# Kernel optimization log

Measured on AMD Instinct MI355X. Metric: run time of the kernel, lower is better.

## Reference

```python
import jax, jax.numpy as jnp
import numpy as np

NUM_HEADS = 12
HEAD_DIM = 64  # d_out // num_heads = 768 // 12


def setup_inputs() -> dict:
    key = jax.random.key(0)
    k1, k2 = jax.random.split(key)
    x = jax.random.normal(k1, (2, 2048, 768), dtype=jnp.float32)
    # torch Linear weight: [d_out, d_in], y = x @ W.T
    Wq = jax.random.normal(k2, (768, 768), dtype=jnp.float32) * 0.02
    return {"x": x, "Wq": Wq}


def reference(x, Wq):
    b, n, d_in = x.shape
    H, hd = NUM_HEADS, HEAD_DIM
    d_out = H * hd
    # NOTE: the original module uses Wq for queries, keys AND values.
    qkv = x @ Wq.T                                   # [b, n, d_out]
    h = qkv.reshape(b, n, H, hd).transpose(0, 2, 1, 3)  # [b, H, n, hd]
    scores = jnp.einsum('bhqd,bhkd->bhqk', h, h)      # [b, H, n, n]
    causal = jnp.triu(jnp.ones((n, n), dtype=bool), k=1)
    scores = jnp.where(causal, -jnp.inf, scores)
    attn = jax.nn.softmax(scores / jnp.sqrt(jnp.float32(hd)), axis=-1)
    ctx = jnp.einsum('bhqk,bhkd->bhqd', attn, h)      # [b, H, n, hd]
    # faithful to source: transpose(-2,-1) -> [b, H, hd, n], then view(b, n, d_out)
    ctx = ctx.transpose(0, 1, 3, 2)
    return ctx.reshape(b, n, d_out)
```

## Files before the change

### kernel.cpp

```cpp
#include <hip/hip_runtime.h>
#include <math.h>

typedef __attribute__((ext_vector_type(8)))  short short8;
typedef __attribute__((ext_vector_type(4)))  float floatx4;
typedef __attribute__((ext_vector_type(16))) float floatx16;

#define MFMA16(a, b, c) __builtin_amdgcn_mfma_f32_16x16x32_bf16(a, b, c, 0, 0, 0)
#define MFMA32(a, b, c) __builtin_amdgcn_mfma_f32_32x32x16_bf16(a, b, c, 0, 0, 0)

constexpr int NSEQ = 2048;
constexpr int DIN  = 768;
constexpr int NH   = 12;
constexpr float QSCALE = 0.18033688011112042f;

constexpr int PK = 72;

__device__ __forceinline__ ushort f2bf(float f) {
    unsigned u = __float_as_uint(f);
    u += 0x7FFF + ((u >> 16) & 1);
    return (ushort)(u >> 16);
}
__device__ __forceinline__ float bf2f(ushort u) {
    return __uint_as_float(((unsigned)u) << 16);
}
__device__ __forceinline__ unsigned cvt_pk_bf16(float lo, float hi) {
    unsigned r;
    asm("v_cvt_pk_bf16_f32 %0, %1, %2" : "=v"(r) : "v"(lo), "v"(hi));
    return r;
}
__device__ __forceinline__ short8 pk8(float4 a, float4 b) {
    union { unsigned u[4]; short8 s; } r;
    r.u[0] = cvt_pk_bf16(a.x, a.y);
    r.u[1] = cvt_pk_bf16(a.z, a.w);
    r.u[2] = cvt_pk_bf16(b.x, b.y);
    r.u[3] = cvt_pk_bf16(b.z, b.w);
    return r.s;
}
__device__ __forceinline__ void bar_lds() {
    asm volatile("s_waitcnt lgkmcnt(0)" ::: "memory");
    __builtin_amdgcn_s_barrier();
}

__global__ __launch_bounds__(256, 3)
void qkv_mfma(const float* __restrict__ x, const float* __restrict__ Wq,
              ushort* __restrict__ h)
{
    __shared__ ushort As[2][64 * PK];
    __shared__ ushort Bs[2][64 * PK];

    const int tid  = threadIdx.x;
    const int w    = tid >> 6;
    const int lane = tid & 63;
    const int m    = lane & 15;
    const int quad = lane >> 4;
    const int r0   = blockIdx.x * 64;
    const int c0   = blockIdx.y * 64;
    const int mrow0 = (w & 1) * 32;
    const int ncol0 = (w >> 1) * 32;

    const int srow = tid >> 3;
    const int scol = (tid & 7) * 8;

    floatx4 C[2][2] = {};
    float4 arf[2][2], brf[2][2];

    #pragma unroll
    for (int i = 0; i < 2; ++i) {
        const float* ax = x  + (size_t)(r0 + srow + i * 32) * DIN + scol;
        const float* bx = Wq + (size_t)(c0 + srow + i * 32) * DIN + scol;
        arf[i][0] = ((const float4*)ax)[0]; arf[i][1] = ((const float4*)ax)[1];
        brf[i][0] = ((const float4*)bx)[0]; brf[i][1] = ((const float4*)bx)[1];
    }
    #pragma unroll
    for (int i = 0; i < 2; ++i) {
        *(short8*)&As[0][(srow + i * 32) * PK + scol] = pk8(arf[i][0], arf[i][1]);
        *(short8*)&Bs[0][(srow + i * 32) * PK + scol] = pk8(brf[i][0], brf[i][1]);
    }
    #pragma unroll
    for (int i = 0; i < 2; ++i) {
        const float* ax = x  + (size_t)(r0 + srow + i * 32) * DIN + 64 + scol;
        const float* bx = Wq + (size_t)(c0 + srow + i * 32) * DIN + 64 + scol;
        arf[i][0] = ((const float4*)ax)[0]; arf[i][1] = ((const float4*)ax)[1];
        brf[i][0] = ((const float4*)bx)[0]; brf[i][1] = ((const float4*)bx)[1];
    }
    bar_lds();

    for (int kk = 0; kk < 12; ++kk) {
        const int cur = kk & 1;

        #pragma unroll
        for (int kt2 = 0; kt2 < 2; ++kt2) {
            short8 a0 = *(const short8*)&As[cur][(mrow0 + m)      * PK + kt2 * 32 + quad * 8];
            short8 a1 = *(const short8*)&As[cur][(mrow0 + 16 + m) * PK + kt2 * 32 + quad * 8];
            short8 b0 = *(const short8*)&Bs[cur][(ncol0 + m)      * PK + kt2 * 32 + quad * 8];
            short8 b1 = *(const short8*)&Bs[cur][(ncol0 + 16 + m) * PK + kt2 * 32 + quad * 8];
            C[0][0] = MFMA16(a0, b0, C[0][0]);
            C[0][1] = MFMA16(a0, b1, C[0][1]);
            C[1][0] = MFMA16(a1, b0, C[1][0]);
            C[1][1] = MFMA16(a1, b1, C[1][1]);
        }

        if (kk + 1 < 12) {
            const int nxt = cur ^ 1;
            #pragma unroll
            for (int i = 0; i < 2; ++i) {
                *(short8*)&As[nxt][(srow + i * 32) * PK + scol] = pk8(arf[i][0], arf[i][1]);
                *(short8*)&Bs[nxt][(srow + i * 32) * PK + scol] = pk8(brf[i][0], brf[i][1]);
            }
            if (kk + 2 < 12) {
                const int k0 = (kk + 2) * 64;
                #pragma unroll
                for (int i = 0; i < 2; ++i) {
                    const float* ax = x  + (size_t)(r0 + srow + i * 32) * DIN + k0 + scol;
                    const float* bx = Wq + (size_t)(c0 + srow + i * 32) * DIN + k0 + scol;
                    arf[i][0] = ((const float4*)ax)[0]; arf[i][1] = ((const float4*)ax)[1];
                    brf[i][0] = ((const float4*)bx)[0]; brf[i][1] = ((const float4*)bx)[1];
                }
            }
            bar_lds();
        }
    }

    #pragma unroll
    for (int mt = 0; mt < 2; ++mt)
        #pragma unroll
        for (int nt = 0; nt < 2; ++nt) {
            int cg = c0 + ncol0 + nt * 16 + m;
            int head = cg >> 6, d = cg & 63;
            #pragma unroll
            for (int r = 0; r < 4; ++r) {
                int rg = r0 + mrow0 + mt * 16 + quad * 4 + r;
                int b = rg >> 11, q = rg & 2047;
                h[((size_t)(b * NH + head) * NSEQ + q) * 64 + d] = f2bf(C[mt][nt][r]);
            }
        }
}

__global__ __launch_bounds__(128, 3)
void attn_mfma(const ushort* __restrict__ h, float* __restrict__ out)
{
    __shared__ ushort Ks[64 * PK];
    __shared__ ushort Vt[64 * PK];

    const int tid  = threadIdx.x;
    const int w    = tid >> 6;
    const int lane = tid & 63;
    const int col  = lane & 31;
    const int hi   = lane >> 5;

    const int xi = blockIdx.x;
    const int bh = blockIdx.y;
    const int qt = ((bh >> 2) & 1) ? xi : (63 - xi);
    const int q0 = qt * 32;
    const int nkt = (qt >> 1) + 1;
    const ushort* __restrict__ Hh = h + (size_t)bh * NSEQ * 64;

    const int kp = (tid & 15) * 4;
    const int cc = tid >> 4;

    short8 qa[4];
    #pragma unroll
    for (int s = 0; s < 4; ++s) {
        short8 raw = *(const short8*)(Hh + (size_t)(q0 + col) * 64 + s * 16 + hi * 8);
        #pragma unroll
        for (int j = 0; j < 8; ++j)
            qa[s][j] = (short)f2bf(bf2f((ushort)raw[j]) * QSCALE);
    }

    floatx16 O[2] = {};
    float lacc = 0.0f;

    short8 fr[4];
#define PREFETCH(KT) do {                                                      \
    const ushort* s_ = Hh + ((size_t)(KT) * 64 + kp) * 64 + cc * 8;            \
    fr[0] = *(const short8*)s_;                                                \
    fr[1] = *(const short8*)(s_ + 64);                                         \
    fr[2] = *(const short8*)(s_ + 128);                                        \
    fr[3] = *(const short8*)(s_ + 192);                                        \
} while (0)

    PREFETCH(0);

    for (int kt = 0; kt < nkt; ++kt) {
        bar_lds();

        #pragma unroll
        for (int j = 0; j < 4; ++j) {
            int ky = kp + j;
            *(short8*)&Ks[ky * PK + (((cc + 2 * (ky & 7)) & 7) << 3)] = fr[j];
        }
        {
            union { short8 v; ushort u[8]; } f0, f1, f2, f3;
            f0.v = fr[0]; f1.v = fr[1]; f2.v = fr[2]; f3.v = fr[3];
            #pragma unroll
            for (int i = 0; i < 8; ++i) {
                uint2 dw;
                dw.x = (unsigned)f0.u[i] | ((unsigned)f1.u[i] << 16);
                dw.y = (unsigned)f2.u[i] | ((unsigned)f3.u[i] << 16);
                *(uint2*)&Vt[(cc * 8 + i) * PK + kp] = dw;
            }
        }
        if (kt + 1 < nkt) PREFETCH(kt + 1);
        bar_lds();

        floatx16 S = {};
        #pragma unroll
        for (int s = 0; s < 4; ++s) {
            int key = w * 32 + col;
            short8 ka = *(const short8*)
                &Ks[key * PK + (((s * 2 + hi + 2 * (col & 7)) & 7) << 3)];
            S = MFMA32(ka, qa[s], S);
        }

        const bool diag = (kt == nkt - 1);
        const int kbase = kt * 64 + w * 32;
        const int qabs  = q0 + col;
        unsigned bfr[2][4];
        #pragma unroll
        for (int h2 = 0; h2 < 2; ++h2) {
            float p[8];
            #pragma unroll
            for (int j = 0; j < 8; ++j) {
                const int reg = h2 * 8 + j;
                const int kl  = (reg & 3) + 8 * (reg >> 2) + 4 * hi;
                float pv = exp2f(S[reg]);
                if (diag && (kbase + kl > qabs)) pv = 0.0f;
                p[j] = pv;
                lacc += pv;
            }
            unsigned a0 = cvt_pk_bf16(p[0], p[1]);
            unsigned a1 = cvt_pk_bf16(p[2], p[3]);
            unsigned a2 = cvt_pk_bf16(p[4], p[5]);
            unsigned a3 = cvt_pk_bf16(p[6], p[7]);
            asm volatile("v_permlane32_swap_b32 %0, %1" : "+v"(a0), "+v"(a2));
            asm volatile("v_permlane32_swap_b32 %0, %1" : "+v"(a1), "+v"(a3));
            bfr[h2][0] = a0; bfr[h2][1] = a1; bfr[h2][2] = a2; bfr[h2][3] = a3;
        }

        #pragma unroll
        for (int h2 = 0; h2 < 2; ++h2) {
            union { unsigned u[4]; short8 v; } pb;
            pb.u[0] = bfr[h2][0]; pb.u[1] = bfr[h2][1];
            pb.u[2] = bfr[h2][2]; pb.u[3] = bfr[h2][3];
            #pragma unroll
            for (int dt = 0; dt < 2; ++dt) {
                short8 va = *(const short8*)
                    &Vt[(dt * 32 + col) * PK + w * 32 + h2 * 16 + hi * 8];
                O[dt] = MFMA32(va, pb.v, O[dt]);
            }
        }
    }
#undef PREFETCH

    lacc += __shfl_xor(lacc, 32);

    float* OmA = (float*)&Ks[0];
    float* OmB = OmA + 32 * 33;
    float* Lg  = OmB + 32 * 33;

    bar_lds();
    {
        float* Om = (w == 0) ? OmA : OmB;
        #pragma unroll
        for (int reg = 0; reg < 16; ++reg) {
            const int dl = (reg & 3) + 8 * (reg >> 2) + 4 * hi;
            Om[dl * 33 + col] = (w == 0) ? O[1][reg] : O[0][reg];
        }
        if (hi == 0) Lg[w * 32 + col] = lacc;
    }
    bar_lds();
    {
        const float linv = 1.0f / (Lg[col] + Lg[32 + col]);
        float* Om = (w == 0) ? OmB : OmA;
        #pragma unroll
        for (int reg = 0; reg < 16; ++reg) {
            const int dl = (reg & 3) + 8 * (reg >> 2) + 4 * hi;
            const int d  = w * 32 + dl;
            const float v = ((w == 0) ? O[0][reg] : O[1][reg]) + Om[dl * 33 + col];
            out[((size_t)bh * 64 + d) * NSEQ + q0 + col] = v * linv;
        }
    }
}

extern "C" void kernel_launch(void* const* d_in, const int* in_sizes, int n_in,
                              void* d_out, int out_size, void* d_ws, size_t ws_size,
                              hipStream_t stream)
{
    (void)in_sizes; (void)n_in; (void)out_size; (void)ws_size;
    const float* x  = (const float*)d_in[0];
    const float* Wq = (const float*)d_in[1];
    float* out = (float*)d_out;

    ushort* hb = (ushort*)d_ws;

    qkv_mfma<<<dim3(64, 12), dim3(256), 0, stream>>>(x, Wq, hb);
    attn_mfma<<<dim3(64, 24), dim3(128), 0, stream>>>(hb, out);
}
```

Baseline: 119.6 us.

## Pair causal query tiles per block and widen key tiles to 128

Each attention block now processes two query tiles (qt and 63-qt) in sequence, so every block gets the same total causal work, and the grid shrinks to 32x24. Key tiles grow from 64 to 128 rows, so each warp computes two 32-key sub-tiles per iteration, with new swizzled LDS layouts for K and transposed V (PV stride 136). The cross-warp reduction at the end is rewritten so warp 1 hands its partial output to warp 0, which does the final normalization. The aim is to balance load and halve barrier and LDS fill overhead per key. In exchange LDS use roughly doubles, which may lower occupancy, and there are half as many blocks.

After: 144.4 us. +20.7%, slower.

```diff
diff --git a/kernel.cpp b/kernel.cpp
--- a/kernel.cpp
+++ b/kernel.cpp
@@ -14,6 +14,7 @@
 constexpr float QSCALE = 0.18033688011112042f;
 
 constexpr int PK = 72;
+constexpr int PV = 136;
 
 __device__ __forceinline__ ushort f2bf(float f) {
     unsigned u = __float_as_uint(f);
@@ -139,8 +140,8 @@
 __global__ __launch_bounds__(128, 3)
 void attn_mfma(const ushort* __restrict__ h, float* __restrict__ out)
 {
-    __shared__ ushort Ks[64 * PK];
-    __shared__ ushort Vt[64 * PK];
+    __shared__ ushort Ks[128 * PK];
+    __shared__ ushort Vt[64 * PV];
 
     const int tid  = threadIdx.x;
     const int w    = tid >> 6;
@@ -148,138 +149,164 @@
     const int col  = lane & 31;
     const int hi   = lane >> 5;
 
-    const int xi = blockIdx.x;
+    const int p  = blockIdx.x;
     const int bh = blockIdx.y;
-    const int qt = ((bh >> 2) & 1) ? xi : (63 - xi);
-    const int q0 = qt * 32;
-    const int nkt = (qt >> 1) + 1;
     const ushort* __restrict__ Hh = h + (size_t)bh * NSEQ * 64;
 
-    const int kp = (tid & 15) * 4;
-    const int cc = tid >> 4;
-
-    short8 qa[4];
-    #pragma unroll
-    for (int s = 0; s < 4; ++s) {
-        short8 raw = *(const short8*)(Hh + (size_t)(q0 + col) * 64 + s * 16 + hi * 8);
-        #pragma unroll
-        for (int j = 0; j < 8; ++j)
-            qa[s][j] = (short)f2bf(bf2f((ushort)raw[j]) * QSCALE);
-    }
-
-    floatx16 O[2] = {};
-    float lacc = 0.0f;
-
-    short8 fr[4];
-#define PREFETCH(KT) do {                                                      \
-    const ushort* s_ = Hh + ((size_t)(KT) * 64 + kp) * 64 + cc * 8;            \
-    fr[0] = *(const short8*)s_;                                                \
-    fr[1] = *(const short8*)(s_ + 64);                                         \
-    fr[2] = *(const short8*)(s_ + 128);                                        \
-    fr[3] = *(const short8*)(s_ + 192);                                        \
+    const int kr4 = (tid & 31) * 4;
+    const int dbb = (tid >> 5) * 2;
+    const int rg4 = (kr4 >> 3) & 3;
+    const int csw0 = ((dbb     + 2 * rg4) & 7) * 8;
+    const int csw1 = ((dbb + 1 + 2 * rg4) & 7) * 8;
+    const int kb   = kr4 >> 3;
+    const int koff = kr4 & 7;
+    const int kbp0 = ((kb + 2 * ((dbb)     & 3)) & 15) * 8 + koff;
+    const int kbp1 = ((kb + 2 * ((dbb + 1) & 3)) & 15) * 8 + koff;
+
+    const int swadd = 2 * (col >> 3);
+
+    float* Om = (float*)&Ks[0];
+    float* Lg = (float*)&Vt[0];
+
+    short8 fr[4][2];
+#define PRE(KT) do {                                                           \
+    _Pragma("unroll")                                                          \
+    for (int j = 0; j < 4; ++j) {                                              \
+        const ushort* s_ = Hh + ((size_t)(KT) * 128 + kr4 + j) * 64 + dbb * 8; \
+        fr[j][0] = *(const short8*)s_;                                         \
+        fr[j][1] = *(const short8*)(s_ + 8);                                   \
+    }                                                                          \
 } while (0)
 
-    PREFETCH(0);
-
-    for (int kt = 0; kt < nkt; ++kt) {
-        bar_lds();
-
-        #pragma unroll
-        for (int j = 0; j < 4; ++j) {
-            int ky = kp + j;
-            *(short8*)&Ks[ky * PK + (((cc + 2 * (ky & 7)) & 7) << 3)] = fr[j];
-        }
-        {
-            union { short8 v; ushort u[8]; } f0, f1, f2, f3;
-            f0.v = fr[0]; f1.v = fr[1]; f2.v = fr[2]; f3.v = fr[3];
-            #pragma unroll
-            for (int i = 0; i < 8; ++i) {
-                uint2 dw;
-                dw.x = (unsigned)f0.u[i] | ((unsigned)f1.u[i] << 16);
-                dw.y = (unsigned)f2.u[i] | ((unsigned)f3.u[i] << 16);
-                *(uint2*)&Vt[(cc * 8 + i) * PK + kp] = dw;
-            }
-        }
-        if (kt + 1 < nkt) PREFETCH(kt + 1);
-        bar_lds();
-
-        floatx16 S = {};
+    #pragma unroll 1
+    for (int half = 0; half < 2; ++half) {
+        if (half) bar_lds();
+
+        const int qt  = half ? p : (63 - p);
+        const int q0  = qt * 32;
+        const int nkt = (qt + 4) >> 2;
+
+        short8 qa[4];
         #pragma unroll
         for (int s = 0; s < 4; ++s) {
-            int key = w * 32 + col;
-            short8 ka = *(const short8*)
-                &Ks[key * PK + (((s * 2 + hi + 2 * (col & 7)) & 7) << 3)];
-            S = MFMA32(ka, qa[s], S);
-        }
-
-        const bool diag = (kt == nkt - 1);
-        const int kbase = kt * 64 + w * 32;
-        const int qabs  = q0 + col;
-        unsigned bfr[2][4];
-        #pragma unroll
-        for (int h2 = 0; h2 < 2; ++h2) {
-            float p[8];
-            #pragma unroll
-            for (int j = 0; j < 8; ++j) {
-                const int reg = h2 * 8 + j;
-                const int kl  = (reg & 3) + 8 * (reg >> 2) + 4 * hi;
-                float pv = exp2f(S[reg]);
-                if (diag && (kbase + kl > qabs)) pv = 0.0f;
-                p[j] = pv;
-                lacc += pv;
-            }
-            unsigned a0 = cvt_pk_bf16(p[0], p[1]);
-            unsigned a1 = cvt_pk_bf16(p[2], p[3]);
-            unsigned a2 = cvt_pk_bf16(p[4], p[5]);
-            unsigned a3 = cvt_pk_bf16(p[6], p[7]);
-            asm volatile("v_permlane32_swap_b32 %0, %1" : "+v"(a0), "+v"(a2));
-            asm volatile("v_permlane32_swap_b32 %0, %1" : "+v"(a1), "+v"(a3));
-            bfr[h2][0] = a0; bfr[h2][1] = a1; bfr[h2][2] = a2; bfr[h2][3] = a3;
-        }
-
-        #pragma unroll
-        for (int h2 = 0; h2 < 2; ++h2) {
-            union { unsigned u[4]; short8 v; } pb;
-            pb.u[0] = bfr[h2][0]; pb.u[1] = bfr[h2][1];
-            pb.u[2] = bfr[h2][2]; pb.u[3] = bfr[h2][3];
-            #pragma unroll
-            for (int dt = 0; dt < 2; ++dt) {
-                short8 va = *(const short8*)
-                    &Vt[(dt * 32 + col) * PK + w * 32 + h2 * 16 + hi * 8];
-                O[dt] = MFMA32(va, pb.v, O[dt]);
-            }
-        }
-    }
-#undef PREFETCH
-
-    lacc += __shfl_xor(lacc, 32);
-
-    float* OmA = (float*)&Ks[0];
-    float* OmB = OmA + 32 * 33;
-    float* Lg  = OmB + 32 * 33;
-
-    bar_lds();
-    {
-        float* Om = (w == 0) ? OmA : OmB;
-        #pragma unroll
-        for (int reg = 0; reg < 16; ++reg) {
-            const int dl = (reg & 3) + 8 * (reg >> 2) + 4 * hi;
-            Om[dl * 33 + col] = (w == 0) ? O[1][reg] : O[0][reg];
-        }
-        if (hi == 0) Lg[w * 32 + col] = lacc;
-    }
-    bar_lds();
-    {
-        const float linv = 1.0f / (Lg[col] + Lg[32 + col]);
-        float* Om = (w == 0) ? OmB : OmA;
-        #pragma unroll
-        for (int reg = 0; reg < 16; ++reg) {
-            const int dl = (reg & 3) + 8 * (reg >> 2) + 4 * hi;
-            const int d  = w * 32 + dl;
-            const float v = ((w == 0) ? O[0][reg] : O[1][reg]) + Om[dl * 33 + col];
-            out[((size_t)bh * 64 + d) * NSEQ + q0 + col] = v * linv;
-        }
-    }
+            short8 raw = *(const short8*)(Hh + (size_t)(q0 + col) * 64 + s * 16 + hi * 8);
+            #pragma unroll
+            for (int j = 0; j < 8; ++j)
+                qa[s][j] = (short)f2bf(bf2f((ushort)raw[j]) * QSCALE);
+        }
+
+        floatx16 O[2] = {};
+        float lacc = 0.0f;
+
+        PRE(0);
+
+        for (int kt = 0; kt < nkt; ++kt) {
+            bar_lds();
+
+            #pragma unroll
+            for (int j = 0; j < 4; ++j) {
+                *(short8*)&Ks[(kr4 + j) * PK + csw0] = fr[j][0];
+                *(short8*)&Ks[(kr4 + j) * PK + csw1] = fr[j][1];
+            }
+            {
+                union { short8 v; ushort u[8]; } f[4][2];
+                #pragma unroll
+                for (int j = 0; j < 4; ++j) { f[j][0].v = fr[j][0]; f[j][1].v = fr[j][1]; }
+                #pragma unroll
+                for (int b = 0; b < 2; ++b) {
+                    const int kcol = b ? kbp1 : kbp0;
+                    #pragma unroll
+                    for (int i = 0; i < 8; ++i) {
+                        uint2 dw;
+                        dw.x = (unsigned)f[0][b].u[i] | ((unsigned)f[1][b].u[i] << 16);
+                        dw.y = (unsigned)f[2][b].u[i] | ((unsigned)f[3][b].u[i] << 16);
+                        *(uint2*)&Vt[((dbb + b) * 8 + i) * PV + kcol] = dw;
+                    }
+                }
+            }
+            if (kt + 1 < nkt) PRE(kt + 1);
+            bar_lds();
+
+            #pragma unroll
+            for (int sub = 0; sub < 2; ++sub) {
+                floatx16 S = {};
+                const int key = w * 64 + sub * 32 + col;
+                #pragma unroll
+                for (int s = 0; s < 4; ++s) {
+                    short8 ka = *(const short8*)
+                        &Ks[key * PK + (((2 * s + hi) + swadd) & 7) * 8];
+                    S = MFMA32(ka, qa[s], S);
+                }
+
+                const bool diag = (kt == nkt - 1);
+                const int kbase = kt * 128 + w * 64 + sub * 32;
+                const int qabs  = q0 + col;
+                unsigned bfr[2][4];
+                #pragma unroll
+                for (int h2 = 0; h2 < 2; ++h2) {
+                    float pv[8];
+                    #pragma unroll
+                    for (int j = 0; j < 8; ++j) {
+                        const int reg = h2 * 8 + j;
+                        const int kl  = (reg & 3) + 8 * (reg >> 2) + 4 * hi;
+                        float e = exp2f(S[reg]);
+                        if (diag && (kbase + kl > qabs)) e = 0.0f;
+                        pv[j] = e;
+                        lacc += e;
+                    }
+                    unsigned a0 = cvt_pk_bf16(pv[0], pv[1]);
+                    unsigned a1 = cvt_pk_bf16(pv[2], pv[3]);
+                    unsigned a2 = cvt_pk_bf16(pv[4], pv[5]);
+                    unsigned a3 = cvt_pk_bf16(pv[6], pv[7]);
+                    asm volatile("v_permlane32_swap_b32 %0, %1" : "+v"(a0), "+v"(a2));
+                    asm volatile("v_permlane32_swap_b32 %0, %1" : "+v"(a1), "+v"(a3));
+                    bfr[h2][0] = a0; bfr[h2][1] = a1; bfr[h2][2] = a2; bfr[h2][3] = a3;
+                }
+
+                #pragma unroll
+                for (int h2 = 0; h2 < 2; ++h2) {
+                    union { unsigned u[4]; short8 v; } pb;
+                    pb.u[0] = bfr[h2][0]; pb.u[1] = bfr[h2][1];
+                    pb.u[2] = bfr[h2][2]; pb.u[3] = bfr[h2][3];
+                    const int kbv = ((8 * w + 4 * sub + 2 * h2 + hi) + swadd) & 15;
+                    #pragma unroll
+                    for (int dt = 0; dt < 2; ++dt) {
+                        short8 va = *(const short8*)
+                            &Vt[(dt * 32 + col) * PV + kbv * 8];
+                        O[dt] = MFMA32(va, pb.v, O[dt]);
+                    }
+                }
+            }
+        }
+
+        lacc += __shfl_xor(lacc, 32);
+
+        bar_lds();
+        if (w == 1) {
+            #pragma unroll
+            for (int dt = 0; dt < 2; ++dt)
+                #pragma unroll
+                for (int reg = 0; reg < 16; ++reg) {
+                    const int dl = (reg & 3) + 8 * (reg >> 2) + 4 * hi;
+                    Om[(dt * 32 + dl) * 33 + col] = O[dt][reg];
+                }
+            if (hi == 0) Lg[col] = lacc;
+        }
+        bar_lds();
+        if (w == 0) {
+            const float linv = 1.0f / (lacc + Lg[col]);
+            #pragma unroll
+            for (int dt = 0; dt < 2; ++dt)
+                #pragma unroll
+                for (int reg = 0; reg < 16; ++reg) {
+                    const int dl = (reg & 3) + 8 * (reg >> 2) + 4 * hi;
+                    const int d  = dt * 32 + dl;
+                    const float v = O[dt][reg] + Om[d * 33 + col];
+                    out[((size_t)bh * 64 + d) * NSEQ + q0 + col] = v * linv;
+                }
+        }
+    }
+#undef PRE
 }
 
 extern "C" void kernel_launch(void* const* d_in, const int* in_sizes, int n_in,
@@ -294,5 +321,5 @@
     ushort* hb = (ushort*)d_ws;
 
     qkv_mfma<<<dim3(64, 12), dim3(256), 0, stream>>>(x, Wq, hb);
-    attn_mfma<<<dim3(64, 24), dim3(128), 0, stream>>>(hb, out);
-}
+    attn_mfma<<<dim3(32, 24), dim3(128), 0, stream>>>(hb, out);
+}
```
